# Kernel tuning notes

Hardware: AMD Instinct MI355X
Metric: run time of the kernel (lower is better)

Reference implementation:

```python
import jax, jax.numpy as jnp
import numpy as np


def setup_inputs() -> dict:
    key = jax.random.key(0)
    x = jax.random.normal(key, (32, 1, 1024, 1024), dtype=jnp.float32)
    return {"x": x}


def reference(x) -> jnp.ndarray:
    # Original torch loop computes a running max down the height dim (dim=2)
    # for channel 0 (C=1 here), overwriting each element with the prefix max.
    # This is exactly a cumulative-max (prefix-max scan) along axis=2.
    return jax.lax.associative_scan(jnp.maximum, x, axis=2)
```

## Files before the change

kernel.cpp:

```cpp
#include <hip/hip_runtime.h>


constexpr int B = 32;
constexpr int H = 1024;
constexpr int W = 1024;
constexpr int ROW4 = W / 4;
constexpr int SW4 = 8;
constexpr int NSTRIP = ROW4 / SW4;
constexpr int CH = 128;
constexpr int NCHUNK = H / CH;
constexpr int R = 4;

__device__ __forceinline__ float4 max4(float4 a, float4 b) {
    return make_float4(fmaxf(a.x, b.x), fmaxf(a.y, b.y),
                       fmaxf(a.z, b.z), fmaxf(a.w, b.w));
}

__device__ __forceinline__ float4 shflup4(float4 v, int d) {
    float4 r;
    r.x = __shfl_up(v.x, d, 64);
    r.y = __shfl_up(v.y, d, 64);
    r.z = __shfl_up(v.z, d, 64);
    r.w = __shfl_up(v.w, d, 64);
    return r;
}

__global__ __launch_bounds__(256) void cummax_sp(const float* __restrict__ xf,
                                                 float* __restrict__ of) {
    __shared__ float4 wavetot[2][32];

    const int tid = threadIdx.x;
    const int lane = tid & 63;
    const int wid = tid >> 6;
    const int w = tid & 7;
    const int hsegG = tid >> 3;
    const int hseg_l = (tid >> 3) & 7;

    const int b = blockIdx.x >> 5;
    const int strip = blockIdx.x & (NSTRIP - 1);
    const float4* x4 = (const float4*)xf;
    float4* o4 = (float4*)of;
    const size_t tbase = (size_t)b * (H * ROW4) + (size_t)strip * SW4 + w;

    const float ninf = -__builtin_inff();
    const float4 ninf4 = make_float4(ninf, ninf, ninf, ninf);
    float4 carry = ninf4;

    float4 cur[R], nxt[R];

#pragma unroll
    for (int r = 0; r < R; ++r)
        cur[r] = x4[tbase + (size_t)(hsegG * R + r) * ROW4];

#pragma unroll
    for (int c = 0; c < NCHUNK; ++c) {
        if (c + 1 < NCHUNK) {
#pragma unroll
            for (int r = 0; r < R; ++r)
                nxt[r] = x4[tbase + (size_t)((c + 1) * CH + hsegG * R + r) * ROW4];
        }

        float4 m = max4(max4(cur[0], cur[1]), max4(cur[2], cur[3]));

        float4 incl = m;
        { float4 t = shflup4(incl, 8);  if (lane >= 8)  incl = max4(incl, t); }
        { float4 t = shflup4(incl, 16); if (lane >= 16) incl = max4(incl, t); }
        { float4 t = shflup4(incl, 32); if (lane >= 32) incl = max4(incl, t); }
        float4 ew = shflup4(incl, 8);
        float4 excl = (hseg_l == 0) ? ninf4 : ew;

        if (hseg_l == 7) wavetot[c & 1][wid * 8 + w] = incl;
        __syncthreads();

        float4 crosspre = carry;
        float4 tot = carry;
#pragma unroll
        for (int w2 = 0; w2 < 4; ++w2) {
            float4 v = wavetot[c & 1][w2 * 8 + w];
            if (w2 < wid) crosspre = max4(crosspre, v);
            tot = max4(tot, v);
        }
        carry = tot;

        float4 a = max4(crosspre, excl);
#pragma unroll
        for (int r = 0; r < R; ++r) {
            a = max4(a, cur[r]);
            o4[tbase + (size_t)(c * CH + hsegG * R + r) * ROW4] = a;
        }

        if (c + 1 < NCHUNK) {
#pragma unroll
            for (int r = 0; r < R; ++r) cur[r] = nxt[r];
        }
    }
}

extern "C" void kernel_launch(void* const* d_in, const int* in_sizes, int n_in,
                              void* d_out, int out_size, void* d_ws, size_t ws_size,
                              hipStream_t stream) {
    const float* x = (const float*)d_in[0];
    float* out = (float*)d_out;
    cummax_sp<<<B * NSTRIP, 256, 0, stream>>>(x, out);
}
```

Before: 242.3 us.

## Replace block-level scan with independent per-wave column scans

Each wavefront now scans a 4-float4-wide strip over the full height on its own, using warp shuffles only. This removes the shared-memory exchange and __syncthreads between the four waves. Each lane now prefetches 8 rows instead of 4, for more memory-level parallelism. In exchange, each row segment is 64 bytes, which may reduce coalescing efficiency, and the grid has half as many blocks.

New measurement: 274.7 us. +13.4%, slower.

```diff
diff --git a/kernel.cpp b/kernel.cpp
--- a/kernel.cpp
+++ b/kernel.cpp
@@ -5,11 +5,14 @@
 constexpr int H = 1024;
 constexpr int W = 1024;
 constexpr int ROW4 = W / 4;
-constexpr int SW4 = 8;
+constexpr int SW4 = 4;
 constexpr int NSTRIP = ROW4 / SW4;
-constexpr int CH = 128;
+constexpr int NSEG = 64 / SW4;
+constexpr int R = 8;
+constexpr int CH = NSEG * R;
 constexpr int NCHUNK = H / CH;
-constexpr int R = 4;
+constexpr int WPB = 4;
+constexpr int NBLK = B * NSTRIP / WPB;
 
 __device__ __forceinline__ float4 max4(float4 a, float4 b) {
     return make_float4(fmaxf(a.x, b.x), fmaxf(a.y, b.y),
@@ -25,19 +28,25 @@
     return r;
 }
 
-__global__ __launch_bounds__(256) void cummax_sp(const float* __restrict__ xf,
-                                                 float* __restrict__ of) {
-    __shared__ float4 wavetot[2][32];
+__device__ __forceinline__ float4 shfl4(float4 v, int src) {
+    float4 r;
+    r.x = __shfl(v.x, src, 64);
+    r.y = __shfl(v.y, src, 64);
+    r.z = __shfl(v.z, src, 64);
+    r.w = __shfl(v.w, src, 64);
+    return r;
+}
 
-    const int tid = threadIdx.x;
-    const int lane = tid & 63;
-    const int wid = tid >> 6;
-    const int w = tid & 7;
-    const int hsegG = tid >> 3;
-    const int hseg_l = (tid >> 3) & 7;
+__global__ __launch_bounds__(256) void cummax_wave(const float* __restrict__ xf,
+                                                   float* __restrict__ of) {
+    const int lane = threadIdx.x & 63;
+    const int wid = threadIdx.x >> 6;
+    const int gid = blockIdx.x * WPB + wid;
+    const int b = gid >> 6;
+    const int strip = gid & (NSTRIP - 1);
+    const int w = lane & (SW4 - 1);
+    const int hseg = lane >> 2;
 
-    const int b = blockIdx.x >> 5;
-    const int strip = blockIdx.x & (NSTRIP - 1);
     const float4* x4 = (const float4*)xf;
     float4* o4 = (float4*)of;
     const size_t tbase = (size_t)b * (H * ROW4) + (size_t)strip * SW4 + w;
@@ -50,43 +59,38 @@
 
 #pragma unroll
     for (int r = 0; r < R; ++r)
-        cur[r] = x4[tbase + (size_t)(hsegG * R + r) * ROW4];
+        cur[r] = x4[tbase + (size_t)(hseg * R + r) * ROW4];
 
 #pragma unroll
     for (int c = 0; c < NCHUNK; ++c) {
         if (c + 1 < NCHUNK) {
 #pragma unroll
             for (int r = 0; r < R; ++r)
-                nxt[r] = x4[tbase + (size_t)((c + 1) * CH + hsegG * R + r) * ROW4];
+                nxt[r] = x4[tbase + (size_t)((c + 1) * CH + hseg * R + r) * ROW4];
         }
 
-        float4 m = max4(max4(cur[0], cur[1]), max4(cur[2], cur[3]));
+        float4 m = cur[0];
+#pragma unroll
+        for (int r = 1; r < R; ++r) m = max4(m, cur[r]);
 
         float4 incl = m;
+        { float4 t = shflup4(incl, 4);  if (lane >= 4)  incl = max4(incl, t); }
         { float4 t = shflup4(incl, 8);  if (lane >= 8)  incl = max4(incl, t); }
         { float4 t = shflup4(incl, 16); if (lane >= 16) incl = max4(incl, t); }
         { float4 t = shflup4(incl, 32); if (lane >= 32) incl = max4(incl, t); }
-        float4 ew = shflup4(incl, 8);
-        float4 excl = (hseg_l == 0) ? ninf4 : ew;
 
-        if (hseg_l == 7) wavetot[c & 1][wid * 8 + w] = incl;
-        __syncthreads();
+        float4 ew = shflup4(incl, 4);
+        float4 pre = carry;
+        if (hseg != 0) pre = max4(pre, ew);
 
-        float4 crosspre = carry;
-        float4 tot = carry;
-#pragma unroll
-        for (int w2 = 0; w2 < 4; ++w2) {
-            float4 v = wavetot[c & 1][w2 * 8 + w];
-            if (w2 < wid) crosspre = max4(crosspre, v);
-            tot = max4(tot, v);
-        }
-        carry = tot;
+        float4 tot = shfl4(incl, 60 + w);
+        carry = max4(carry, tot);
 
-        float4 a = max4(crosspre, excl);
+        float4 a = pre;
 #pragma unroll
         for (int r = 0; r < R; ++r) {
             a = max4(a, cur[r]);
-            o4[tbase + (size_t)(c * CH + hsegG * R + r) * ROW4] = a;
+            o4[tbase + (size_t)(c * CH + hseg * R + r) * ROW4] = a;
         }
 
         if (c + 1 < NCHUNK) {
@@ -101,5 +105,5 @@
                               hipStream_t stream) {
     const float* x = (const float*)d_in[0];
     float* out = (float*)d_out;
-    cummax_sp<<<B * NSTRIP, 256, 0, stream>>>(x, out);
+    cummax_wave<<<NBLK, 256, 0, stream>>>(x, out);
 }
```

## Split column cummax into two-pass segment reduce-then-scan using workspace

Applied to the files above, without the earlier changes.

Replaces the single-pass strip kernel with a two-kernel reduce-then-scan. The first kernel computes per-segment column maxima into workspace, and the second combines the preceding segment totals as a carry and rescans each segment. It also remaps block indices in the apply pass. This removes the in-block shuffle and barrier scan and the serial chunk chain, but reads the input twice, adding about 128MB of extra traffic plus a second launch. The old kernel is kept as a fallback when the workspace is too small.

After: 259.3 us. +7.0%, slower.

```diff
diff --git a/kernel.cpp b/kernel.cpp
--- a/kernel.cpp
+++ b/kernel.cpp
@@ -5,16 +5,86 @@
 constexpr int H = 1024;
 constexpr int W = 1024;
 constexpr int ROW4 = W / 4;
-constexpr int SW4 = 8;
-constexpr int NSTRIP = ROW4 / SW4;
-constexpr int CH = 128;
-constexpr int NCHUNK = H / CH;
-constexpr int R = 4;
+constexpr int NSEG = 32;
+constexpr int SH = H / NSEG;
+constexpr int NB = B * NSEG;
+constexpr size_t TOT_BYTES = (size_t)NB * ROW4 * sizeof(float4);
 
 __device__ __forceinline__ float4 max4(float4 a, float4 b) {
     return make_float4(fmaxf(a.x, b.x), fmaxf(a.y, b.y),
                        fmaxf(a.z, b.z), fmaxf(a.w, b.w));
 }
+
+__global__ __launch_bounds__(256) void seg_colmax(const float* __restrict__ xf,
+                                                  float* __restrict__ tf) {
+    const int id = blockIdx.x;
+    const int b = id >> 5;
+    const int s = id & (NSEG - 1);
+    const int t = threadIdx.x;
+    const float4* x4 = (const float4*)xf;
+    float4* t4 = (float4*)tf;
+
+    const size_t base = ((size_t)b * H + (size_t)s * SH) * ROW4 + t;
+    const float ninf = -__builtin_inff();
+    float4 m = make_float4(ninf, ninf, ninf, ninf);
+
+#pragma unroll
+    for (int g = 0; g < SH; g += 8) {
+        float4 v[8];
+#pragma unroll
+        for (int r = 0; r < 8; ++r) v[r] = x4[base + (size_t)(g + r) * ROW4];
+#pragma unroll
+        for (int r = 0; r < 8; ++r) m = max4(m, v[r]);
+    }
+    t4[(size_t)id * ROW4 + t] = m;
+}
+
+__global__ __launch_bounds__(256) void seg_apply(const float* __restrict__ xf,
+                                                 const float* __restrict__ tf,
+                                                 float* __restrict__ of) {
+    const int id0 = blockIdx.x;
+    const int id = (id0 & 7) * (NB / 8) + (id0 >> 3);
+    const int b = id >> 5;
+    const int s = id & (NSEG - 1);
+    const int t = threadIdx.x;
+    const float4* x4 = (const float4*)xf;
+    const float4* t4 = (const float4*)tf;
+    float4* o4 = (float4*)of;
+
+    const float ninf = -__builtin_inff();
+    float4 carry = make_float4(ninf, ninf, ninf, ninf);
+
+#pragma unroll
+    for (int g = 0; g < NSEG; g += 8) {
+        float4 v[8];
+#pragma unroll
+        for (int k = 0; k < 8; ++k)
+            v[k] = t4[(size_t)(b * NSEG + g + k) * ROW4 + t];
+#pragma unroll
+        for (int k = 0; k < 8; ++k)
+            if (g + k < s) carry = max4(carry, v[k]);
+    }
+
+    const size_t base = ((size_t)b * H + (size_t)s * SH) * ROW4 + t;
+    float4 m = carry;
+#pragma unroll
+    for (int g = 0; g < SH; g += 8) {
+        float4 v[8];
+#pragma unroll
+        for (int r = 0; r < 8; ++r) v[r] = x4[base + (size_t)(g + r) * ROW4];
+#pragma unroll
+        for (int r = 0; r < 8; ++r) {
+            m = max4(m, v[r]);
+            o4[base + (size_t)(g + r) * ROW4] = m;
+        }
+    }
+}
+
+constexpr int F_SW4 = 8;
+constexpr int F_NSTRIP = ROW4 / F_SW4;
+constexpr int F_CH = 128;
+constexpr int F_NCHUNK = H / F_CH;
+constexpr int F_R = 4;
 
 __device__ __forceinline__ float4 shflup4(float4 v, int d) {
     float4 r;
@@ -28,50 +98,40 @@
 __global__ __launch_bounds__(256) void cummax_sp(const float* __restrict__ xf,
                                                  float* __restrict__ of) {
     __shared__ float4 wavetot[2][32];
-
     const int tid = threadIdx.x;
     const int lane = tid & 63;
     const int wid = tid >> 6;
     const int w = tid & 7;
     const int hsegG = tid >> 3;
     const int hseg_l = (tid >> 3) & 7;
-
     const int b = blockIdx.x >> 5;
-    const int strip = blockIdx.x & (NSTRIP - 1);
+    const int strip = blockIdx.x & (F_NSTRIP - 1);
     const float4* x4 = (const float4*)xf;
     float4* o4 = (float4*)of;
-    const size_t tbase = (size_t)b * (H * ROW4) + (size_t)strip * SW4 + w;
-
+    const size_t tbase = (size_t)b * (H * ROW4) + (size_t)strip * F_SW4 + w;
     const float ninf = -__builtin_inff();
     const float4 ninf4 = make_float4(ninf, ninf, ninf, ninf);
     float4 carry = ninf4;
-
-    float4 cur[R], nxt[R];
-
+    float4 cur[F_R], nxt[F_R];
 #pragma unroll
-    for (int r = 0; r < R; ++r)
-        cur[r] = x4[tbase + (size_t)(hsegG * R + r) * ROW4];
-
+    for (int r = 0; r < F_R; ++r)
+        cur[r] = x4[tbase + (size_t)(hsegG * F_R + r) * ROW4];
 #pragma unroll
-    for (int c = 0; c < NCHUNK; ++c) {
-        if (c + 1 < NCHUNK) {
+    for (int c = 0; c < F_NCHUNK; ++c) {
+        if (c + 1 < F_NCHUNK) {
 #pragma unroll
-            for (int r = 0; r < R; ++r)
-                nxt[r] = x4[tbase + (size_t)((c + 1) * CH + hsegG * R + r) * ROW4];
+            for (int r = 0; r < F_R; ++r)
+                nxt[r] = x4[tbase + (size_t)((c + 1) * F_CH + hsegG * F_R + r) * ROW4];
         }
-
         float4 m = max4(max4(cur[0], cur[1]), max4(cur[2], cur[3]));
-
         float4 incl = m;
         { float4 t = shflup4(incl, 8);  if (lane >= 8)  incl = max4(incl, t); }
         { float4 t = shflup4(incl, 16); if (lane >= 16) incl = max4(incl, t); }
         { float4 t = shflup4(incl, 32); if (lane >= 32) incl = max4(incl, t); }
         float4 ew = shflup4(incl, 8);
         float4 excl = (hseg_l == 0) ? ninf4 : ew;
-
         if (hseg_l == 7) wavetot[c & 1][wid * 8 + w] = incl;
         __syncthreads();
-
         float4 crosspre = carry;
         float4 tot = carry;
 #pragma unroll
@@ -81,17 +141,15 @@
             tot = max4(tot, v);
         }
         carry = tot;
-
         float4 a = max4(crosspre, excl);
 #pragma unroll
-        for (int r = 0; r < R; ++r) {
+        for (int r = 0; r < F_R; ++r) {
             a = max4(a, cur[r]);
-            o4[tbase + (size_t)(c * CH + hsegG * R + r) * ROW4] = a;
+            o4[tbase + (size_t)(c * F_CH + hsegG * F_R + r) * ROW4] = a;
         }
-
-        if (c + 1 < NCHUNK) {
+        if (c + 1 < F_NCHUNK) {
 #pragma unroll
-            for (int r = 0; r < R; ++r) cur[r] = nxt[r];
+            for (int r = 0; r < F_R; ++r) cur[r] = nxt[r];
         }
     }
 }
@@ -101,5 +159,11 @@
                               hipStream_t stream) {
     const float* x = (const float*)d_in[0];
     float* out = (float*)d_out;
-    cummax_sp<<<B * NSTRIP, 256, 0, stream>>>(x, out);
+    if (ws_size >= TOT_BYTES && d_ws != nullptr) {
+        float* tot = (float*)d_ws;
+        seg_colmax<<<NB, 256, 0, stream>>>(x, tot);
+        seg_apply<<<NB, 256, 0, stream>>>(x, tot, out);
+    } else {
+        cummax_sp<<<B * F_NSTRIP, 256, 0, stream>>>(x, out);
+    }
 }
```
